# Kernel optimization log

Hardware: AMD Instinct MI355X
Metric: run time of the kernel (lower is better)

The kernel has to match this reference:

```python
import jax, jax.numpy as jnp
import numpy as np

C = 8          # n_features
D = 256        # grid side
N = 1_000_000  # query points
K = 27         # kernel**3 neighborhood
OUTPUT_SCALE = 1.0


def _linear_params(key, fin, fout):
    kw, kb = jax.random.split(key)
    s = 1.0 / np.sqrt(fin)
    W = jax.random.uniform(kw, (fin, fout), jnp.float32, -s, s)
    b = jax.random.uniform(kb, (fout,), jnp.float32, -s, s)
    return W, b


def setup_inputs() -> dict:
    key = jax.random.key(0)
    ks = jax.random.split(key, 10)
    points = jax.random.uniform(ks[0], (N, 3), jnp.float32, 0.0, float(D - 1))
    grid = jax.random.normal(ks[1], (1, C, D, D, D), dtype=jnp.float32)
    Wc, bc = _linear_params(ks[2], K * C, C)
    W1, b1 = _linear_params(ks[3], 2 * C, 32)
    W2, b2 = _linear_params(ks[4], C + 32, 16)
    W3, b3 = _linear_params(ks[5], C + 16, 8)
    W4, b4 = _linear_params(ks[6], C + 8, C)
    Ws, bs = _linear_params(ks[7], C, 1)
    Wo, bo = _linear_params(ks[8], C, 1)
    return dict(points=points, grid=grid, Wc=Wc, bc=bc, W1=W1, b1=b1,
                W2=W2, b2=b2, W3=W3, b3=b3, W4=W4, b4=b4,
                Ws=Ws, bs=bs, Wo=Wo, bo=bo)


def _layernorm(z):
    # elementwise_affine=False, eps=1e-5, over last dim
    m = jnp.mean(z, axis=-1, keepdims=True)
    v = jnp.var(z, axis=-1, keepdims=True)
    return (z - m) * jax.lax.rsqrt(v + 1e-5)


def reference(points, grid, Wc, bc, W1, b1, W2, b2, W3, b3, W4, b4, Ws, bs, Wo, bo):
    act = jnp.tanh  # config.RENDERER.activation = torch.nn.Tanh()
    pad = 1  # kernel // 2
    # ReplicationPad3d on (1,C,D,H,W)
    g = jnp.pad(grid[0], ((0, 0), (pad, pad), (pad, pad), (pad, pad)), mode='edge')  # (C, D+2, D+2, D+2)
    pts = points + pad
    idx = jnp.floor(pts).astype(jnp.int32)  # (N,3)
    # 27-neighborhood offsets in loop order i,j,k in range(-1,2)
    r = jnp.arange(-1, 2)
    off = jnp.stack(jnp.meshgrid(r, r, r, indexing='ij'), axis=-1).reshape(K, 3)
    nb = idx[:, None, :] + off[None].astype(jnp.int32)  # (N,27,3)
    feat = g[:, nb[..., 0], nb[..., 1], nb[..., 2]]  # (C, N, 27)
    feat = jnp.transpose(feat, (1, 2, 0))            # (N, 27, C) point-major, neighbor, channel
    cen = g[:, idx[:, 0], idx[:, 1], idx[:, 2]].T    # (N, C)
    # use_count_renderer: normalize last channel (count) by global max
    max_count = jnp.maximum(jnp.max(feat[..., -1]), jnp.max(cen[:, -1])) + 1e-9
    feat = jnp.concatenate([feat[..., :-1], feat[..., -1:] / max_count], axis=-1)
    cen = jnp.concatenate([cen[:, :-1], cen[:, -1:] / max_count], axis=-1)
    x = feat.reshape(feat.shape[0], K * C)  # matches torch contiguous view (neighbor-then-channel)
    # DenseNet-style tiny MLP chain (Dropout2d is identity in eval)
    ctx = act(_layernorm(x @ Wc + bc))
    h = act(jnp.concatenate([cen, ctx], axis=1) @ W1 + b1)
    h = act(jnp.concatenate([cen, h], axis=1) @ W2 + b2)
    h = act(jnp.concatenate([cen, h], axis=1) @ W3 + b3)
    h = act(jnp.concatenate([cen, h], axis=1) @ W4 + b4)
    sdf = OUTPUT_SCALE * jnp.tanh(h @ Ws + bs)
    occ = jax.nn.sigmoid(h @ Wo + bo)
    return jnp.concatenate([sdf, occ], axis=1)  # (N, 2)
```

## Files before the change

### kernel.cpp

```cpp
#include <hip/hip_runtime.h>
#include <hip/hip_fp16.h>

typedef unsigned int u32;
typedef unsigned short u16;

__device__ __forceinline__ u32 encf(float f){ u32 u=__float_as_uint(f); return (u&0x80000000u)? ~u : (u|0x80000000u); }
__device__ __forceinline__ float decf(u32 u){ return (u&0x80000000u)? __uint_as_float(u&0x7fffffffu) : __uint_as_float(~u); }

__device__ __forceinline__ float fast_tanh(float x){
  x = fminf(fmaxf(x, -15.f), 15.f);
  float e = __expf(2.f*x);
  return (e - 1.f) * __builtin_amdgcn_rcpf(e + 1.f);
}
__device__ __forceinline__ float fast_sigmoid(float x){
  x = fminf(fmaxf(x, -15.f), 15.f);
  return __builtin_amdgcn_rcpf(1.f + __expf(-x));
}

__device__ __forceinline__ int base_ix(float p){
  return (int)floorf(p + 1.0f) - 1;
}

__global__ __launch_bounds__(256) void repack16(const float* __restrict__ g,
                                                uint4* __restrict__ rg,
                                                u16* __restrict__ zy){
  u32 v = blockIdx.x*256u + threadIdx.x;
  float c0 = g[v];
  float c1 = g[(1u<<24)+v];
  float c2 = g[(2u<<24)+v];
  float c3 = g[(3u<<24)+v];
  float c4 = g[(4u<<24)+v];
  float c5 = g[(5u<<24)+v];
  float c6 = g[(6u<<24)+v];
  float c7 = g[(7u<<24)+v];
  __half2 p0 = __floats2half2_rn(c0,c1);
  __half2 p1 = __floats2half2_rn(c2,c3);
  __half2 p2 = __floats2half2_rn(c4,c5);
  __half2 p3 = __floats2half2_rn(c6,c7);
  uint4 o;
  o.x = *(const u32*)&p0; o.y = *(const u32*)&p1;
  o.z = *(const u32*)&p2; o.w = *(const u32*)&p3;
  rg[v] = o;
  u32 z = v & 255u;
  u32 y = (v>>8) & 255u;
  const float* g7 = g + ((size_t)7u<<24);
  u32 zm = (z==0u)? v : v-1u;
  u32 zp = (z==255u)? v : v+1u;
  float m = -3.0e38f;
  #pragma unroll
  for (int dy=-1; dy<=1; ++dy){
    int yy = (int)y + dy;
    u32 ro = (yy<0 || yy>255) ? 0u : (u32)(dy*256);
    u32 b0 = zm + ro, b1 = v + ro, b2 = zp + ro;
    m = fmaxf(m, fmaxf(g7[b0], fmaxf(g7[b1], g7[b2])));
  }
  zy[v] = __half_as_ushort(__float2half_rn(m));
}

__global__ __launch_bounds__(256) void xdil(const u16* __restrict__ zy,
                                            u16* __restrict__ xd){
  u32 v = blockIdx.x*256u + threadIdx.x;
  u32 x = v>>16;
  float a = __half2float(__ushort_as_half(zy[x==0u   ? v : v-65536u]));
  float b = __half2float(__ushort_as_half(zy[v]));
  float c = __half2float(__ushort_as_half(zy[x==255u ? v : v+65536u]));
  float m = fmaxf(a, fmaxf(b, c));
  xd[v] = __half_as_ushort(__float2half_rn(m));
}

__device__ __forceinline__ u32 cell_id(int ix, int iy, int iz){
  return ((u32)(ix>>3)<<10) | ((u32)(iy>>3)<<5) | (u32)(iz>>3);
}

__global__ __launch_bounds__(256) void hist(const float* __restrict__ pts,
                                            u32* __restrict__ cnt, int n){
  for (int i = blockIdx.x*blockDim.x + threadIdx.x; i < n; i += gridDim.x*blockDim.x){
    int ix = base_ix(pts[3*i]);
    int iy = base_ix(pts[3*i+1]);
    int iz = base_ix(pts[3*i+2]);
    atomicAdd(&cnt[cell_id(ix,iy,iz)], 1u);
  }
}

__global__ __launch_bounds__(1024) void scan32k(const u32* __restrict__ cnt,
                                                u32* __restrict__ ofs){
  __shared__ u32 sums[1024];
  int t = threadIdx.x;
  u32 loc[32];
  u32 s = 0;
  #pragma unroll
  for (int k=0;k<32;k++){ loc[k] = cnt[t*32+k]; s += loc[k]; }
  sums[t] = s;
  __syncthreads();
  for (int off=1; off<1024; off<<=1){
    u32 v = (t>=off)? sums[t-off] : 0u;
    __syncthreads();
    sums[t] += v;
    __syncthreads();
  }
  u32 run = (t>0)? sums[t-1] : 0u;
  #pragma unroll
  for (int k=0;k<32;k++){ ofs[t*32+k] = run; run += loc[k]; }
}

__global__ __launch_bounds__(256) void scatter(const float* __restrict__ pts,
                                               u32* __restrict__ ofs,
                                               float4* __restrict__ srt, int n){
  for (int i = blockIdx.x*blockDim.x + threadIdx.x; i < n; i += gridDim.x*blockDim.x){
    float px = pts[3*i], py = pts[3*i+1], pz = pts[3*i+2];
    int ix = base_ix(px), iy = base_ix(py), iz = base_ix(pz);
    u32 r = atomicAdd(&ofs[cell_id(ix,iy,iz)], 1u);
    srt[r] = make_float4(px, py, pz, __uint_as_float((u32)i));
  }
}

__global__ __launch_bounds__(256) void kmax_pt(const float4* __restrict__ srt,
                                               const u16* __restrict__ xd,
                                               u32* __restrict__ wmax, int n){
  __shared__ float red[4];
  float m = -3.0e38f;
  for (int i = blockIdx.x*blockDim.x + threadIdx.x; i < n; i += gridDim.x*blockDim.x){
    float4 rec = srt[i];
    int ix = base_ix(rec.x);
    int iy = base_ix(rec.y);
    int iz = base_ix(rec.z);
    u32 cb = ((u32)ix<<16) | ((u32)iy<<8) | (u32)iz;
    m = fmaxf(m, __half2float(__ushort_as_half(xd[cb])));
  }
  #pragma unroll
  for (int o=32;o>=1;o>>=1) m = fmaxf(m, __shfl_xor(m, o));
  int wid = threadIdx.x >> 6;
  if ((threadIdx.x & 63)==0) red[wid] = m;
  __syncthreads();
  if (threadIdx.x == 0){
    float r = fmaxf(fmaxf(red[0],red[1]), fmaxf(red[2],red[3]));
    atomicMax(wmax, encf(r));
  }
}

__device__ __forceinline__ void mlp_tail(const float* __restrict__ cen,
                                         const float* __restrict__ acc0,
                                         float2* __restrict__ out, int i,
                                         const float* __restrict__ W1, const float* __restrict__ b1,
                                         const float* __restrict__ W2, const float* __restrict__ b2,
                                         const float* __restrict__ W3, const float* __restrict__ b3,
                                         const float* __restrict__ W4, const float* __restrict__ b4,
                                         const float* __restrict__ Ws, const float* __restrict__ bs,
                                         const float* __restrict__ Wo, const float* __restrict__ bo)
{
  float mean = 0.f;
  #pragma unroll
  for (int j=0;j<8;j++) mean += acc0[j];
  mean *= 0.125f;
  float var = 0.f;
  #pragma unroll
  for (int j=0;j<8;j++){ float t = acc0[j]-mean; var += t*t; }
  var *= 0.125f;
  float rs = rsqrtf(var + 1e-5f);
  float ctx[8];
  #pragma unroll
  for (int j=0;j<8;j++) ctx[j] = fast_tanh((acc0[j]-mean)*rs);

  float h1[32];
  #pragma unroll
  for (int j=0;j<32;j++){
    float s = b1[j];
    #pragma unroll
    for (int c=0;c<8;c++) s = fmaf(cen[c], W1[c*32 + j], s);
    #pragma unroll
    for (int c=0;c<8;c++) s = fmaf(ctx[c], W1[(8+c)*32 + j], s);
    h1[j] = fast_tanh(s);
  }
  float h2[16];
  #pragma unroll
  for (int j=0;j<16;j++){
    float s = b2[j];
    #pragma unroll
    for (int c=0;c<8;c++) s = fmaf(cen[c], W2[c*16 + j], s);
    #pragma unroll
    for (int c=0;c<32;c++) s = fmaf(h1[c], W2[(8+c)*16 + j], s);
    h2[j] = fast_tanh(s);
  }
  float h3[8];
  #pragma unroll
  for (int j=0;j<8;j++){
    float s = b3[j];
    #pragma unroll
    for (int c=0;c<8;c++) s = fmaf(cen[c], W3[c*8 + j], s);
    #pragma unroll
    for (int c=0;c<16;c++) s = fmaf(h2[c], W3[(8+c)*8 + j], s);
    h3[j] = fast_tanh(s);
  }
  float h4[8];
  #pragma unroll
  for (int j=0;j<8;j++){
    float s = b4[j];
    #pragma unroll
    for (int c=0;c<8;c++) s = fmaf(cen[c], W4[c*8 + j], s);
    #pragma unroll
    for (int c=0;c<8;c++) s = fmaf(h3[c], W4[(8+c)*8 + j], s);
    h4[j] = fast_tanh(s);
  }
  float ssdf = bs[0];
  float socc = bo[0];
  #pragma unroll
  for (int c=0;c<8;c++){
    ssdf = fmaf(h4[c], Ws[c], ssdf);
    socc = fmaf(h4[c], Wo[c], socc);
  }
  out[i] = make_float2(fast_tanh(ssdf), fast_sigmoid(socc));
}

__global__ __launch_bounds__(256) void kmain16(const float4* __restrict__ srt,
                                               const uint4* __restrict__ rg,
                                               const u32* __restrict__ wmax,
                                               float2* __restrict__ out, int n,
                                               const float* __restrict__ Wc, const float* __restrict__ bc,
                                               const float* __restrict__ W1, const float* __restrict__ b1,
                                               const float* __restrict__ W2, const float* __restrict__ b2,
                                               const float* __restrict__ W3, const float* __restrict__ b3,
                                               const float* __restrict__ W4, const float* __restrict__ b4,
                                               const float* __restrict__ Ws, const float* __restrict__ bs,
                                               const float* __restrict__ Wo, const float* __restrict__ bo)
{
  u32 nwg = gridDim.x;
  u32 q = nwg >> 3, r = nwg & 7u;
  u32 xcd = blockIdx.x & 7u, sub = blockIdx.x >> 3;
  u32 bid = (xcd < r ? xcd*(q+1u) : r*(q+1u) + (xcd-r)*q) + sub;

  int j = (int)(bid*256u + threadIdx.x);
  if (j >= n) return;
  float4 rec = srt[j];
  int i = (int)__float_as_uint(rec.w);
  float inv = 1.0f / (decf(*wmax) + 1e-9f);

  int ix = base_ix(rec.x);
  int iy = base_ix(rec.y);
  int iz = base_ix(rec.z);
  int xs[3] = {max(ix-1,0), ix, min(ix+1,255)};
  int ys[3] = {max(iy-1,0), iy, min(iy+1,255)};
  int zs[3] = {max(iz-1,0), iz, min(iz+1,255)};

  float cen[8];
  float acc[8];
  #pragma unroll
  for (int jj=0;jj<8;jj++) acc[jj] = bc[jj];

  #pragma unroll
  for (int a=0;a<3;a++)
  #pragma unroll
  for (int b=0;b<3;b++)
  #pragma unroll
  for (int d=0;d<3;d++){
    const int kk = (a*3+b)*3+d;
    u32 vb = ((u32)xs[a]<<16) | ((u32)ys[b]<<8) | (u32)zs[d];
    uint4 qv = rg[vb];
    float2 f0 = __half22float2(*(const __half2*)&qv.x);
    float2 f1 = __half22float2(*(const __half2*)&qv.y);
    float2 f2 = __half22float2(*(const __half2*)&qv.z);
    float2 f3 = __half22float2(*(const __half2*)&qv.w);
    float v[8] = {f0.x,f0.y,f1.x,f1.y,f2.x,f2.y,f3.x, f3.y*inv};
    if (kk == 13){
      #pragma unroll
      for (int c=0;c<8;c++) cen[c] = v[c];
    }
    #pragma unroll
    for (int c=0;c<8;c++)
      #pragma unroll
      for (int jj=0;jj<8;jj++)
        acc[jj] = fmaf(v[c], Wc[(kk*8+c)*8 + jj], acc[jj]);
  }

  mlp_tail(cen, acc, out, i, W1,b1,W2,b2,W3,b3,W4,b4,Ws,bs,Wo,bo);
}

__global__ __launch_bounds__(256) void kmax_direct(const float* __restrict__ pts,
                                                   const float* __restrict__ g7,
                                                   u32* __restrict__ wmax, int n){
  float m = -3.0e38f;
  for (int i = blockIdx.x*blockDim.x + threadIdx.x; i < n; i += gridDim.x*blockDim.x){
    int ix = base_ix(pts[3*i]);
    int iy = base_ix(pts[3*i+1]);
    int iz = base_ix(pts[3*i+2]);
    int xs[3] = {max(ix-1,0), ix, min(ix+1,255)};
    int ys[3] = {max(iy-1,0), iy, min(iy+1,255)};
    int zs[3] = {max(iz-1,0), iz, min(iz+1,255)};
    #pragma unroll
    for (int a=0;a<3;a++)
    #pragma unroll
    for (int b=0;b<3;b++){
      u32 rb = ((u32)xs[a]<<16) | ((u32)ys[b]<<8);
      #pragma unroll
      for (int d=0;d<3;d++) m = fmaxf(m, g7[rb + (u32)zs[d]]);
    }
  }
  #pragma unroll
  for (int o=32;o>=1;o>>=1) m = fmaxf(m, __shfl_xor(m, o));
  if ((threadIdx.x & 63)==0) atomicMax(wmax, encf(m));
}

__global__ __launch_bounds__(256) void kmain_direct(const float* __restrict__ pts,
                                                    const float* __restrict__ g,
                                                    const u32* __restrict__ wmax,
                                                    float2* __restrict__ out, int n,
                                                    const float* __restrict__ Wc, const float* __restrict__ bc,
                                                    const float* __restrict__ W1, const float* __restrict__ b1,
                                                    const float* __restrict__ W2, const float* __restrict__ b2,
                                                    const float* __restrict__ W3, const float* __restrict__ b3,
                                                    const float* __restrict__ W4, const float* __restrict__ b4,
                                                    const float* __restrict__ Ws, const float* __restrict__ bs,
                                                    const float* __restrict__ Wo, const float* __restrict__ bo)
{
  int i = blockIdx.x*256 + threadIdx.x;
  if (i >= n) return;
  float inv = 1.0f / (decf(*wmax) + 1e-9f);

  int ix = base_ix(pts[3*i]);
  int iy = base_ix(pts[3*i+1]);
  int iz = base_ix(pts[3*i+2]);
  int xs[3] = {max(ix-1,0), ix, min(ix+1,255)};
  int ys[3] = {max(iy-1,0), iy, min(iy+1,255)};
  int zs[3] = {max(iz-1,0), iz, min(iz+1,255)};

  u32 cb = ((u32)ix<<16) | ((u32)iy<<8) | (u32)iz;
  float cen[8];
  #pragma unroll
  for (int c=0;c<8;c++) cen[c] = g[((u32)c<<24) + cb];
  cen[7] *= inv;

  float acc[8];
  #pragma unroll
  for (int j=0;j<8;j++) acc[j] = bc[j];

  #pragma unroll
  for (int a=0;a<3;a++)
  #pragma unroll
  for (int b=0;b<3;b++)
  #pragma unroll
  for (int d=0;d<3;d++){
    const int kk = (a*3+b)*3+d;
    u32 vb = ((u32)xs[a]<<16) | ((u32)ys[b]<<8) | (u32)zs[d];
    float v[8];
    #pragma unroll
    for (int c=0;c<8;c++) v[c] = g[((u32)c<<24) + vb];
    v[7] *= inv;
    #pragma unroll
    for (int c=0;c<8;c++)
      #pragma unroll
      for (int j=0;j<8;j++)
        acc[j] = fmaf(v[c], Wc[(kk*8+c)*8 + j], acc[j]);
  }

  mlp_tail(cen, acc, out, i, W1,b1,W2,b2,W3,b3,W4,b4,Ws,bs,Wo,bo);
}

extern "C" void kernel_launch(void* const* d_in, const int* in_sizes, int n_in,
                              void* d_out, int out_size, void* d_ws, size_t ws_size,
                              hipStream_t stream)
{
  const float* pts  = (const float*)d_in[0];
  const float* grid = (const float*)d_in[1];
  int n = in_sizes[0] / 3;

  const size_t NV       = (size_t)1 << 24;
  const size_t RG_BYTES = NV * 16;
  const size_t SL_BYTES = NV * 2;
  const size_t SRT_BYTES= (size_t)n * 16;
  const size_t CNT_BYTES= 32768 * 4;
  const size_t NEED     = RG_BYTES + 2*SL_BYTES + SRT_BYTES + 2*CNT_BYTES + 64;

  if (ws_size >= NEED){
    char* base = (char*)d_ws;
    uint4*  rg   = (uint4*)base;
    u16*    zy   = (u16*)(base + RG_BYTES);
    u16*    xd   = (u16*)(base + RG_BYTES + SL_BYTES);
    float4* srt  = (float4*)(base + RG_BYTES + 2*SL_BYTES);
    u32*    cnt  = (u32*)(base + RG_BYTES + 2*SL_BYTES + SRT_BYTES);
    u32*    ofs  = (u32*)(base + RG_BYTES + 2*SL_BYTES + SRT_BYTES + CNT_BYTES);
    u32*    wmax = (u32*)(base + RG_BYTES + 2*SL_BYTES + SRT_BYTES + 2*CNT_BYTES);

    hipMemsetAsync(cnt, 0, CNT_BYTES, stream);
    hipMemsetAsync(wmax, 0, 64, stream);
    repack16<<<65536, 256, 0, stream>>>(grid, rg, zy);
    xdil<<<65536, 256, 0, stream>>>(zy, xd);
    hist<<<2048, 256, 0, stream>>>(pts, cnt, n);
    scan32k<<<1, 1024, 0, stream>>>(cnt, ofs);
    scatter<<<2048, 256, 0, stream>>>(pts, ofs, srt, n);
    kmax_pt<<<2048, 256, 0, stream>>>(srt, xd, wmax, n);
    kmain16<<<(n+255)/256, 256, 0, stream>>>(srt, rg, wmax, (float2*)d_out, n,
        (const float*)d_in[2],  (const float*)d_in[3],
        (const float*)d_in[4],  (const float*)d_in[5],
        (const float*)d_in[6],  (const float*)d_in[7],
        (const float*)d_in[8],  (const float*)d_in[9],
        (const float*)d_in[10], (const float*)d_in[11],
        (const float*)d_in[12], (const float*)d_in[13],
        (const float*)d_in[14], (const float*)d_in[15]);
  } else {
    u32* wmax = (u32*)d_ws;
    hipMemsetAsync(wmax, 0, 64, stream);
    kmax_direct<<<2048, 256, 0, stream>>>(pts, grid + ((size_t)7<<24), wmax, n);
    kmain_direct<<<(n+255)/256, 256, 0, stream>>>(pts, grid, wmax, (float2*)d_out, n,
        (const float*)d_in[2],  (const float*)d_in[3],
        (const float*)d_in[4],  (const float*)d_in[5],
        (const float*)d_in[6],  (const float*)d_in[7],
        (const float*)d_in[8],  (const float*)d_in[9],
        (const float*)d_in[10], (const float*)d_in[11],
        (const float*)d_in[12], (const float*)d_in[13],
        (const float*)d_in[14], (const float*)d_in[15]);
  }
}
```

Baseline: 541.7 us.

## Fuse x-dilation into scatter, vectorize grid repack, prefetch 27-neighbor loads

```diff
diff --git a/kernel.cpp b/kernel.cpp
--- a/kernel.cpp
+++ b/kernel.cpp
@@ -23,49 +23,50 @@
 
 __global__ __launch_bounds__(256) void repack16(const float* __restrict__ g,
                                                 uint4* __restrict__ rg,
-                                                u16* __restrict__ zy){
-  u32 v = blockIdx.x*256u + threadIdx.x;
-  float c0 = g[v];
-  float c1 = g[(1u<<24)+v];
-  float c2 = g[(2u<<24)+v];
-  float c3 = g[(3u<<24)+v];
-  float c4 = g[(4u<<24)+v];
-  float c5 = g[(5u<<24)+v];
-  float c6 = g[(6u<<24)+v];
-  float c7 = g[(7u<<24)+v];
-  __half2 p0 = __floats2half2_rn(c0,c1);
-  __half2 p1 = __floats2half2_rn(c2,c3);
-  __half2 p2 = __floats2half2_rn(c4,c5);
-  __half2 p3 = __floats2half2_rn(c6,c7);
-  uint4 o;
-  o.x = *(const u32*)&p0; o.y = *(const u32*)&p1;
-  o.z = *(const u32*)&p2; o.w = *(const u32*)&p3;
-  rg[v] = o;
-  u32 z = v & 255u;
-  u32 y = (v>>8) & 255u;
+                                                ushort4* __restrict__ zy4){
+  u32 t = blockIdx.x*256u + threadIdx.x;
+  u32 v0 = t << 2;
+  const float4* gv = (const float4*)g;
+  float4 C[8];
+  #pragma unroll
+  for (int c=0;c<8;c++) C[c] = gv[((u32)c<<22) + t];
+
+  #pragma unroll
+  for (int k=0;k<4;k++){
+    float a[8];
+    #pragma unroll
+    for (int c=0;c<8;c++) a[c] = ((const float*)&C[c])[k];
+    __half2 p0 = __floats2half2_rn(a[0],a[1]);
+    __half2 p1 = __floats2half2_rn(a[2],a[3]);
+    __half2 p2 = __floats2half2_rn(a[4],a[5]);
+    __half2 p3 = __floats2half2_rn(a[6],a[7]);
+    uint4 o;
+    o.x=*(const u32*)&p0; o.y=*(const u32*)&p1; o.z=*(const u32*)&p2; o.w=*(const u32*)&p3;
+    rg[v0+k]=o;
+  }
+
+  u32 z0 = v0 & 255u;
+  u32 y  = (v0>>8) & 255u;
   const float* g7 = g + ((size_t)7u<<24);
-  u32 zm = (z==0u)? v : v-1u;
-  u32 zp = (z==255u)? v : v+1u;
-  float m = -3.0e38f;
-  #pragma unroll
-  for (int dy=-1; dy<=1; ++dy){
-    int yy = (int)y + dy;
-    u32 ro = (yy<0 || yy>255) ? 0u : (u32)(dy*256);
-    u32 b0 = zm + ro, b1 = v + ro, b2 = zp + ro;
-    m = fmaxf(m, fmaxf(g7[b0], fmaxf(g7[b1], g7[b2])));
-  }
-  zy[v] = __half_as_ushort(__float2half_rn(m));
-}
-
-__global__ __launch_bounds__(256) void xdil(const u16* __restrict__ zy,
-                                            u16* __restrict__ xd){
-  u32 v = blockIdx.x*256u + threadIdx.x;
-  u32 x = v>>16;
-  float a = __half2float(__ushort_as_half(zy[x==0u   ? v : v-65536u]));
-  float b = __half2float(__ushort_as_half(zy[v]));
-  float c = __half2float(__ushort_as_half(zy[x==255u ? v : v+65536u]));
-  float m = fmaxf(a, fmaxf(b, c));
-  xd[v] = __half_as_ushort(__float2half_rn(m));
+  float zmax[4] = {-3.0e38f,-3.0e38f,-3.0e38f,-3.0e38f};
+  #pragma unroll
+  for (int r=0;r<3;r++){
+    int yy = (int)y + r - 1;
+    u32 ro = (yy<0 || yy>255)? v0 : (u32)((int)v0 + (r-1)*256);
+    float4 f = (r==1)? C[7] : *(const float4*)(g7 + ro);
+    float e0 = (z0==0u)?   f.x : g7[ro-1u];
+    float e5 = (z0==252u)? f.w : g7[ro+4u];
+    float e[6] = {e0, f.x, f.y, f.z, f.w, e5};
+    #pragma unroll
+    for (int k=0;k<4;k++)
+      zmax[k] = fmaxf(zmax[k], fmaxf(e[k], fmaxf(e[k+1], e[k+2])));
+  }
+  ushort4 zo;
+  zo.x = __half_as_ushort(__float2half_rn(zmax[0]));
+  zo.y = __half_as_ushort(__float2half_rn(zmax[1]));
+  zo.z = __half_as_ushort(__float2half_rn(zmax[2]));
+  zo.w = __half_as_ushort(__float2half_rn(zmax[3]));
+  zy4[t] = zo;
 }
 
 __device__ __forceinline__ u32 cell_id(int ix, int iy, int iz){
@@ -103,29 +104,24 @@
   for (int k=0;k<32;k++){ ofs[t*32+k] = run; run += loc[k]; }
 }
 
-__global__ __launch_bounds__(256) void scatter(const float* __restrict__ pts,
-                                               u32* __restrict__ ofs,
-                                               float4* __restrict__ srt, int n){
+__global__ __launch_bounds__(256) void scatter_max(const float* __restrict__ pts,
+                                                   u32* __restrict__ ofs,
+                                                   const u16* __restrict__ zy,
+                                                   float4* __restrict__ srt,
+                                                   u32* __restrict__ wmax, int n){
+  __shared__ float red[4];
+  float m = -3.0e38f;
   for (int i = blockIdx.x*blockDim.x + threadIdx.x; i < n; i += gridDim.x*blockDim.x){
     float px = pts[3*i], py = pts[3*i+1], pz = pts[3*i+2];
     int ix = base_ix(px), iy = base_ix(py), iz = base_ix(pz);
     u32 r = atomicAdd(&ofs[cell_id(ix,iy,iz)], 1u);
     srt[r] = make_float4(px, py, pz, __uint_as_float((u32)i));
-  }
-}
-
-__global__ __launch_bounds__(256) void kmax_pt(const float4* __restrict__ srt,
-                                               const u16* __restrict__ xd,
-                                               u32* __restrict__ wmax, int n){
-  __shared__ float red[4];
-  float m = -3.0e38f;
-  for (int i = blockIdx.x*blockDim.x + threadIdx.x; i < n; i += gridDim.x*blockDim.x){
-    float4 rec = srt[i];
-    int ix = base_ix(rec.x);
-    int iy = base_ix(rec.y);
-    int iz = base_ix(rec.z);
     u32 cb = ((u32)ix<<16) | ((u32)iy<<8) | (u32)iz;
-    m = fmaxf(m, __half2float(__ushort_as_half(xd[cb])));
+    u32 xm = (ix==0)? cb : cb - 65536u;
+    float a = __half2float(__ushort_as_half(zy[xm]));
+    float b = __half2float(__ushort_as_half(zy[cb]));
+    float c = __half2float(__ushort_as_half(zy[cb + 65536u]));
+    m = fmaxf(m, fmaxf(a, fmaxf(b, c)));
   }
   #pragma unroll
   for (int o=32;o>=1;o>>=1) m = fmaxf(m, __shfl_xor(m, o));
@@ -133,8 +129,8 @@
   if ((threadIdx.x & 63)==0) red[wid] = m;
   __syncthreads();
   if (threadIdx.x == 0){
-    float r = fmaxf(fmaxf(red[0],red[1]), fmaxf(red[2],red[3]));
-    atomicMax(wmax, encf(r));
+    float r2 = fmaxf(fmaxf(red[0],red[1]), fmaxf(red[2],red[3]));
+    atomicMax(wmax, encf(r2));
   }
 }
 
@@ -211,28 +207,28 @@
   out[i] = make_float2(fast_tanh(ssdf), fast_sigmoid(socc));
 }
 
-__global__ __launch_bounds__(256) void kmain16(const float4* __restrict__ srt,
-                                               const uint4* __restrict__ rg,
-                                               const u32* __restrict__ wmax,
-                                               float2* __restrict__ out, int n,
-                                               const float* __restrict__ Wc, const float* __restrict__ bc,
-                                               const float* __restrict__ W1, const float* __restrict__ b1,
-                                               const float* __restrict__ W2, const float* __restrict__ b2,
-                                               const float* __restrict__ W3, const float* __restrict__ b3,
-                                               const float* __restrict__ W4, const float* __restrict__ b4,
-                                               const float* __restrict__ Ws, const float* __restrict__ bs,
-                                               const float* __restrict__ Wo, const float* __restrict__ bo)
+__global__ __launch_bounds__(256,3) void kmain16(const float4* __restrict__ srt,
+                                                 const uint4* __restrict__ rg,
+                                                 const u32* __restrict__ wmax,
+                                                 float2* __restrict__ out, int n,
+                                                 const float* __restrict__ Wc, const float* __restrict__ bc,
+                                                 const float* __restrict__ W1, const float* __restrict__ b1,
+                                                 const float* __restrict__ W2, const float* __restrict__ b2,
+                                                 const float* __restrict__ W3, const float* __restrict__ b3,
+                                                 const float* __restrict__ W4, const float* __restrict__ b4,
+                                                 const float* __restrict__ Ws, const float* __restrict__ bs,
+                                                 const float* __restrict__ Wo, const float* __restrict__ bo)
 {
   u32 nwg = gridDim.x;
-  u32 q = nwg >> 3, r = nwg & 7u;
+  u32 qq = nwg >> 3, rr = nwg & 7u;
   u32 xcd = blockIdx.x & 7u, sub = blockIdx.x >> 3;
-  u32 bid = (xcd < r ? xcd*(q+1u) : r*(q+1u) + (xcd-r)*q) + sub;
+  u32 bid = (xcd < rr ? xcd*(qq+1u) : rr*(qq+1u) + (xcd-rr)*qq) + sub;
 
   int j = (int)(bid*256u + threadIdx.x);
   if (j >= n) return;
+  float inv = 1.0f / (decf(*wmax) + 1e-9f);
   float4 rec = srt[j];
   int i = (int)__float_as_uint(rec.w);
-  float inv = 1.0f / (decf(*wmax) + 1e-9f);
 
   int ix = base_ix(rec.x);
   int iy = base_ix(rec.y);
@@ -241,29 +237,38 @@
   int ys[3] = {max(iy-1,0), iy, min(iy+1,255)};
   int zs[3] = {max(iz-1,0), iz, min(iz+1,255)};
 
+  uint4 qv[27];
+  #pragma unroll
+  for (int a=0;a<3;a++)
+  #pragma unroll
+  for (int b=0;b<3;b++)
+  #pragma unroll
+  for (int d=0;d<3;d++)
+    qv[(a*3+b)*3+d] = rg[((u32)xs[a]<<16) | ((u32)ys[b]<<8) | (u32)zs[d]];
+
   float cen[8];
+  {
+    uint4 qc = qv[13];
+    float2 f0 = __half22float2(*(const __half2*)&qc.x);
+    float2 f1 = __half22float2(*(const __half2*)&qc.y);
+    float2 f2 = __half22float2(*(const __half2*)&qc.z);
+    float2 f3 = __half22float2(*(const __half2*)&qc.w);
+    cen[0]=f0.x; cen[1]=f0.y; cen[2]=f1.x; cen[3]=f1.y;
+    cen[4]=f2.x; cen[5]=f2.y; cen[6]=f3.x; cen[7]=f3.y*inv;
+  }
+
   float acc[8];
   #pragma unroll
   for (int jj=0;jj<8;jj++) acc[jj] = bc[jj];
 
   #pragma unroll
-  for (int a=0;a<3;a++)
-  #pragma unroll
-  for (int b=0;b<3;b++)
-  #pragma unroll
-  for (int d=0;d<3;d++){
-    const int kk = (a*3+b)*3+d;
-    u32 vb = ((u32)xs[a]<<16) | ((u32)ys[b]<<8) | (u32)zs[d];
-    uint4 qv = rg[vb];
-    float2 f0 = __half22float2(*(const __half2*)&qv.x);
-    float2 f1 = __half22float2(*(const __half2*)&qv.y);
-    float2 f2 = __half22float2(*(const __half2*)&qv.z);
-    float2 f3 = __half22float2(*(const __half2*)&qv.w);
+  for (int kk=0;kk<27;kk++){
+    uint4 q2 = qv[kk];
+    float2 f0 = __half22float2(*(const __half2*)&q2.x);
+    float2 f1 = __half22float2(*(const __half2*)&q2.y);
+    float2 f2 = __half22float2(*(const __half2*)&q2.z);
+    float2 f3 = __half22float2(*(const __half2*)&q2.w);
     float v[8] = {f0.x,f0.y,f1.x,f1.y,f2.x,f2.y,f3.x, f3.y*inv};
-    if (kk == 13){
-      #pragma unroll
-      for (int c=0;c<8;c++) cen[c] = v[c];
-    }
     #pragma unroll
     for (int c=0;c<8;c++)
       #pragma unroll
@@ -367,26 +372,23 @@
   const size_t SL_BYTES = NV * 2;
   const size_t SRT_BYTES= (size_t)n * 16;
   const size_t CNT_BYTES= 32768 * 4;
-  const size_t NEED     = RG_BYTES + 2*SL_BYTES + SRT_BYTES + 2*CNT_BYTES + 64;
+  const size_t NEED     = RG_BYTES + SL_BYTES + SRT_BYTES + 2*CNT_BYTES + 64;
 
   if (ws_size >= NEED){
     char* base = (char*)d_ws;
-    uint4*  rg   = (uint4*)base;
-    u16*    zy   = (u16*)(base + RG_BYTES);
-    u16*    xd   = (u16*)(base + RG_BYTES + SL_BYTES);
-    float4* srt  = (float4*)(base + RG_BYTES + 2*SL_BYTES);
-    u32*    cnt  = (u32*)(base + RG_BYTES + 2*SL_BYTES + SRT_BYTES);
-    u32*    ofs  = (u32*)(base + RG_BYTES + 2*SL_BYTES + SRT_BYTES + CNT_BYTES);
-    u32*    wmax = (u32*)(base + RG_BYTES + 2*SL_BYTES + SRT_BYTES + 2*CNT_BYTES);
+    uint4*   rg   = (uint4*)base;
+    u16*     zy   = (u16*)(base + RG_BYTES);
+    float4*  srt  = (float4*)(base + RG_BYTES + SL_BYTES);
+    u32*     cnt  = (u32*)(base + RG_BYTES + SL_BYTES + SRT_BYTES);
+    u32*     ofs  = (u32*)(base + RG_BYTES + SL_BYTES + SRT_BYTES + CNT_BYTES);
+    u32*     wmax = (u32*)(base + RG_BYTES + SL_BYTES + SRT_BYTES + 2*CNT_BYTES);
 
     hipMemsetAsync(cnt, 0, CNT_BYTES, stream);
     hipMemsetAsync(wmax, 0, 64, stream);
-    repack16<<<65536, 256, 0, stream>>>(grid, rg, zy);
-    xdil<<<65536, 256, 0, stream>>>(zy, xd);
+    repack16<<<16384, 256, 0, stream>>>(grid, rg, (ushort4*)zy);
     hist<<<2048, 256, 0, stream>>>(pts, cnt, n);
     scan32k<<<1, 1024, 0, stream>>>(cnt, ofs);
-    scatter<<<2048, 256, 0, stream>>>(pts, ofs, srt, n);
-    kmax_pt<<<2048, 256, 0, stream>>>(srt, xd, wmax, n);
+    scatter_max<<<2048, 256, 0, stream>>>(pts, ofs, zy, srt, wmax, n);
     kmain16<<<(n+255)/256, 256, 0, stream>>>(srt, rg, wmax, (float2*)d_out, n,
         (const float*)d_in[2],  (const float*)d_in[3],
         (const float*)d_in[4],  (const float*)d_in[5],
```

Measured after the change: 504.3 us. 6.9% less time.
